# Kernel tuning notes

Measured on AMD Instinct MI355X. Metric: run time of the kernel, lower is better.

Reference implementation:

```python
import jax, jax.numpy as jnp
import numpy as np

N_NODES = 50000


def setup_inputs() -> dict:
    key = jax.random.key(0)
    ks = jax.random.split(key, 6)
    L, d = 3, 128
    x = jax.random.normal(ks[0], (N_NODES, d), dtype=jnp.float32)
    edge_index = jax.random.randint(ks[1], (2, 640000), 0, N_NODES, dtype=jnp.int64)
    s = 1.0 / np.sqrt(d)
    W1 = jax.random.normal(ks[2], (L, d, d), dtype=jnp.float32) * s
    W2 = jax.random.normal(ks[3], (L, d, d), dtype=jnp.float32) * s
    b1 = jnp.zeros((L, d), dtype=jnp.float32)
    b2 = jnp.zeros((L, d), dtype=jnp.float32)
    eps = jnp.zeros((L,), dtype=jnp.float32)
    final_w = jax.random.normal(ks[4], (d + L * d, d), dtype=jnp.float32) / np.sqrt(d + L * d)
    final_b = jnp.zeros((d,), dtype=jnp.float32)
    return {"x": x, "edge_index": edge_index, "W1": W1, "b1": b1,
            "W2": W2, "b2": b2, "eps": eps, "final_w": final_w, "final_b": final_b}


def reference(x, edge_index, W1, b1, W2, b2, eps, final_w, final_b):
    src, dst = edge_index[0], edge_index[1]
    num_layers = W1.shape[0]
    xs = [x]
    h = x
    for l in range(num_layers):
        # GINConv: sum-aggregate neighbor features, add (1+eps)*self, then 2-layer MLP
        agg = jax.ops.segment_sum(h[src], dst, num_segments=N_NODES)  # [N, d]
        z = (1.0 + eps[l]) * h + agg
        z = jax.nn.relu(z @ W1[l] + b1[l])
        h = jax.nn.relu(z @ W2[l] + b2[l])
        xs.append(h)
    out = jnp.concatenate(xs, axis=-1)  # [N, in + L*out]
    return out @ final_w + final_b
```

## Files before the change

kernel.cpp:

```cpp
#include <hip/hip_runtime.h>

#define NNODES 50000
#define NEDGES 640000
#define D 128

typedef unsigned short u16;
typedef unsigned int u32;
typedef __bf16 bf16x8 __attribute__((ext_vector_type(8)));
typedef float f32x4 __attribute__((ext_vector_type(4)));
union AB { uint4 u4; bf16x8 f; };

__device__ __forceinline__ u16 f2b(float f) {
    u32 u = __float_as_uint(f);
    return (u16)((u + 0x7fffu + ((u >> 16) & 1u)) >> 16);
}
__device__ __forceinline__ u32 pack2(float lo, float hi) {
    return (u32)f2b(lo) | ((u32)f2b(hi) << 16);
}
__device__ __forceinline__ float blo(u32 v) { return __uint_as_float(v << 16); }
__device__ __forceinline__ float bhi(u32 v) { return __uint_as_float(v & 0xffff0000u); }

__device__ __forceinline__ void acc8(float* a, uint4 v) {
    a[0] += blo(v.x); a[1] += bhi(v.x);
    a[2] += blo(v.y); a[3] += bhi(v.y);
    a[4] += blo(v.z); a[5] += bhi(v.z);
    a[6] += blo(v.w); a[7] += bhi(v.w);
}

__global__ void k_prep(const float* __restrict__ W1, const float* __restrict__ W2,
                       const float* __restrict__ fw, const float* __restrict__ x,
                       const int* __restrict__ dst,
                       u16* __restrict__ wT1, u16* __restrict__ wT2,
                       u16* __restrict__ fwTc, u32* __restrict__ xb,
                       int* __restrict__ cnt, int* __restrict__ epos) {
    int idx = blockIdx.x * 256 + threadIdx.x;
    if (idx < 3 * 16384) {
        int l = idx >> 14, r = idx & 16383, n = r >> 7, k = r & 127;
        wT1[idx] = f2b(W1[l * 16384 + k * 128 + n]);
        wT2[idx] = f2b(W2[l * 16384 + k * 128 + n]);
    }
    if (idx < 4 * 16384) {
        int ch = idx >> 14, r = idx & 16383, n = r >> 7, k = r & 127;
        fwTc[idx] = f2b(fw[(ch * 128 + k) * 128 + n]);
    }
    if (idx < NEDGES) {
        epos[idx] = atomicAdd(&cnt[dst[idx]], 1);
    }
    if (idx < NNODES * 64) {
        float2 v = ((const float2*)x)[idx];
        xb[idx] = pack2(v.x, v.y);
    }
}

__global__ void k_scan1(const int* __restrict__ cnt, int* __restrict__ rp,
                        int* __restrict__ bsum) {
    __shared__ int s[256];
    int tid = threadIdx.x;
    int i = blockIdx.x * 256 + tid;
    int v = (i < NNODES) ? cnt[i] : 0;
    s[tid] = v;
    __syncthreads();
    for (int off = 1; off < 256; off <<= 1) {
        int t = (tid >= off) ? s[tid - off] : 0;
        __syncthreads();
        s[tid] += t;
        __syncthreads();
    }
    if (i < NNODES) rp[i] = s[tid] - v;
    if (tid == 255) bsum[blockIdx.x] = s[255];
}

__global__ void k_scan2(int* __restrict__ bsum, int nb) {
    __shared__ int s[256];
    int tid = threadIdx.x;
    int v = (tid < nb) ? bsum[tid] : 0;
    s[tid] = v;
    __syncthreads();
    for (int off = 1; off < 256; off <<= 1) {
        int t = (tid >= off) ? s[tid - off] : 0;
        __syncthreads();
        s[tid] += t;
        __syncthreads();
    }
    if (tid < nb) bsum[tid] = s[tid] - v;
}

__global__ void k_add(int* __restrict__ rp, const int* __restrict__ bsum) {
    int i = blockIdx.x * 256 + threadIdx.x;
    if (i < NNODES) rp[i] += bsum[blockIdx.x];
    if (i == 0) rp[NNODES] = NEDGES;
}

__global__ void k_scatter(const int* __restrict__ src, const int* __restrict__ dst,
                          const int* __restrict__ rp, const int* __restrict__ epos,
                          int* __restrict__ srcs) {
    int e = blockIdx.x * 256 + threadIdx.x;
    if (e < NEDGES) srcs[rp[dst[e]] + epos[e]] = src[e];
}

__global__ void k_agg(const uint4* __restrict__ h4, const int* __restrict__ rp,
                      const int* __restrict__ srcs, const float* __restrict__ epsp,
                      uint4* __restrict__ z4) {
    int tid = threadIdx.x;
    int c = tid & 15;
    int node = (blockIdx.x * 256 + tid) >> 4;
    int gbase = tid & 48;
    float sc = 1.0f + epsp[0];

    uint4 sv = h4[node * 16 + c];
    float acc[8];
    acc[0] = sc * blo(sv.x); acc[1] = sc * bhi(sv.x);
    acc[2] = sc * blo(sv.y); acc[3] = sc * bhi(sv.y);
    acc[4] = sc * blo(sv.z); acc[5] = sc * bhi(sv.z);
    acc[6] = sc * blo(sv.w); acc[7] = sc * bhi(sv.w);

    int beg = rp[node], end = rp[node + 1];
    for (int base = beg; base < end; base += 16) {
        int n = end - base; if (n > 16) n = 16;
        int myidx = (base + c < end) ? srcs[base + c] : 0;
        int j = 0;
        for (; j + 8 <= n; j += 8) {
            int s0 = __shfl(myidx, gbase + j + 0, 64);
            int s1 = __shfl(myidx, gbase + j + 1, 64);
            int s2 = __shfl(myidx, gbase + j + 2, 64);
            int s3 = __shfl(myidx, gbase + j + 3, 64);
            int s4 = __shfl(myidx, gbase + j + 4, 64);
            int s5 = __shfl(myidx, gbase + j + 5, 64);
            int s6 = __shfl(myidx, gbase + j + 6, 64);
            int s7 = __shfl(myidx, gbase + j + 7, 64);
            uint4 v0 = h4[s0 * 16 + c]; uint4 v1 = h4[s1 * 16 + c];
            uint4 v2 = h4[s2 * 16 + c]; uint4 v3 = h4[s3 * 16 + c];
            uint4 v4 = h4[s4 * 16 + c]; uint4 v5 = h4[s5 * 16 + c];
            uint4 v6 = h4[s6 * 16 + c]; uint4 v7 = h4[s7 * 16 + c];
            acc8(acc, v0); acc8(acc, v1); acc8(acc, v2); acc8(acc, v3);
            acc8(acc, v4); acc8(acc, v5); acc8(acc, v6); acc8(acc, v7);
        }
        for (; j + 4 <= n; j += 4) {
            int s0 = __shfl(myidx, gbase + j + 0, 64);
            int s1 = __shfl(myidx, gbase + j + 1, 64);
            int s2 = __shfl(myidx, gbase + j + 2, 64);
            int s3 = __shfl(myidx, gbase + j + 3, 64);
            uint4 v0 = h4[s0 * 16 + c]; uint4 v1 = h4[s1 * 16 + c];
            uint4 v2 = h4[s2 * 16 + c]; uint4 v3 = h4[s3 * 16 + c];
            acc8(acc, v0); acc8(acc, v1); acc8(acc, v2); acc8(acc, v3);
        }
        for (; j < n; ++j) {
            int s0 = __shfl(myidx, gbase + j, 64);
            uint4 v0 = h4[s0 * 16 + c];
            acc8(acc, v0);
        }
    }

    uint4 o;
    o.x = pack2(acc[0], acc[1]); o.y = pack2(acc[2], acc[3]);
    o.z = pack2(acc[4], acc[5]); o.w = pack2(acc[6], acc[7]);
    z4[node * 16 + c] = o;
}

template <bool FINAL>
__launch_bounds__(256, 2)
__global__ void k_mlp(const u16* __restrict__ A, const u16* __restrict__ wT1g,
                      const float* __restrict__ b1, const u16* __restrict__ wT2g,
                      const float* __restrict__ b2, u16* __restrict__ H,
                      const u16* __restrict__ xbg, const u16* __restrict__ h1g,
                      const u16* __restrict__ h2g, const u16* __restrict__ fwTc,
                      const float* __restrict__ fb, float* __restrict__ out) {
    __shared__ u16 Tb[128 * 128];
    __shared__ u16 wbuf[128 * 128];
    uint4* Tb4 = (uint4*)Tb;
    uint4* wb4 = (uint4*)wbuf;
    int tid = threadIdx.x;
    int r0 = blockIdx.x * 128;
    int wave = tid >> 6, lane = tid & 63, l16 = lane & 15, quad = lane >> 4;

    {
        const uint4* g = (const uint4*)wT1g;
        for (int i = tid; i < 2048; i += 256) {
            int n = i >> 4, ch = i & 15;
            wb4[n * 16 + ((ch + n) & 15)] = g[i];
        }
    }

    AB a[2][4];
#pragma unroll
    for (int s = 0; s < 2; ++s) {
        int row = r0 + wave * 32 + s * 16 + l16;
#pragma unroll
        for (int kb = 0; kb < 4; ++kb) {
            if (row < NNODES)
                a[s][kb].u4 = *(const uint4*)&A[row * 128 + kb * 32 + quad * 8];
            else
                a[s][kb].u4 = make_uint4(0, 0, 0, 0);
        }
    }
    __syncthreads();

    f32x4 acc[2][8];
#pragma unroll
    for (int col = 0; col < 8; ++col) {
        float bv = b1[col * 16 + l16];
        acc[0][col] = (f32x4){bv, bv, bv, bv};
        acc[1][col] = (f32x4){bv, bv, bv, bv};
    }
#pragma unroll
    for (int col = 0; col < 8; ++col) {
#pragma unroll
        for (int kb = 0; kb < 4; ++kb) {
            AB b;
            int n = col * 16 + l16;
            b.u4 = wb4[n * 16 + ((kb * 4 + quad + n) & 15)];
            acc[0][col] = __builtin_amdgcn_mfma_f32_16x16x32_bf16(a[0][kb].f, b.f, acc[0][col], 0, 0, 0);
            acc[1][col] = __builtin_amdgcn_mfma_f32_16x16x32_bf16(a[1][kb].f, b.f, acc[1][col], 0, 0, 0);
        }
    }

#pragma unroll
    for (int s = 0; s < 2; ++s)
#pragma unroll
        for (int col = 0; col < 8; ++col)
#pragma unroll
            for (int r = 0; r < 4; ++r) {
                int row = wave * 32 + s * 16 + quad * 4 + r;
                int kcol = col * 16 + l16;
                int ch = kcol >> 3;
                Tb[row * 128 + ((ch + row) & 15) * 8 + (kcol & 7)] =
                    f2b(fmaxf(acc[s][col][r], 0.f));
            }
    __syncthreads();

    {
        const uint4* g = (const uint4*)wT2g;
        for (int i = tid; i < 2048; i += 256) {
            int n = i >> 4, ch = i & 15;
            wb4[n * 16 + ((ch + n) & 15)] = g[i];
        }
    }
    AB a2[2][4];
#pragma unroll
    for (int s = 0; s < 2; ++s) {
        int m = wave * 32 + s * 16 + l16;
#pragma unroll
        for (int kb = 0; kb < 4; ++kb)
            a2[s][kb].u4 = Tb4[m * 16 + ((kb * 4 + quad + m) & 15)];
    }
    __syncthreads();

#pragma unroll
    for (int col = 0; col < 8; ++col) {
        float bv = b2[col * 16 + l16];
        acc[0][col] = (f32x4){bv, bv, bv, bv};
        acc[1][col] = (f32x4){bv, bv, bv, bv};
    }
#pragma unroll
    for (int col = 0; col < 8; ++col) {
#pragma unroll
        for (int kb = 0; kb < 4; ++kb) {
            AB b;
            int n = col * 16 + l16;
            b.u4 = wb4[n * 16 + ((kb * 4 + quad + n) & 15)];
            acc[0][col] = __builtin_amdgcn_mfma_f32_16x16x32_bf16(a2[0][kb].f, b.f, acc[0][col], 0, 0, 0);
            acc[1][col] = __builtin_amdgcn_mfma_f32_16x16x32_bf16(a2[1][kb].f, b.f, acc[1][col], 0, 0, 0);
        }
    }

#pragma unroll
    for (int s = 0; s < 2; ++s)
#pragma unroll
        for (int col = 0; col < 8; ++col)
#pragma unroll
            for (int r = 0; r < 4; ++r) {
                int row = wave * 32 + s * 16 + quad * 4 + r;
                int kcol = col * 16 + l16;
                int ch = kcol >> 3;
                Tb[row * 128 + ((ch + row) & 15) * 8 + (kcol & 7)] =
                    f2b(fmaxf(acc[s][col][r], 0.f));
            }

    if constexpr (!FINAL) {
        __syncthreads();
        for (int i = tid; i < 2048; i += 256) {
            int r = i >> 4, ch = i & 15;
            int grow = r0 + r;
            if (grow < NNODES)
                *(uint4*)&H[grow * 128 + ch * 8] = Tb4[r * 16 + ((ch + r) & 15)];
        }
    } else {
#pragma unroll
        for (int col = 0; col < 8; ++col) {
            float bv = fb[col * 16 + l16];
            acc[0][col] = (f32x4){bv, bv, bv, bv};
            acc[1][col] = (f32x4){bv, bv, bv, bv};
        }
        const u16* chin[3] = {xbg, h1g, h2g};
        for (int chn = 0; chn < 4; ++chn) {
            __syncthreads();
            {
                const uint4* g = (const uint4*)(fwTc + chn * 16384);
                for (int i = tid; i < 2048; i += 256) {
                    int n = i >> 4, ch = i & 15;
                    wb4[n * 16 + ((ch + n) & 15)] = g[i];
                }
            }
            AB af[2][4];
            if (chn < 3) {
                const u16* cp = chin[chn];
#pragma unroll
                for (int s = 0; s < 2; ++s) {
                    int row = r0 + wave * 32 + s * 16 + l16;
#pragma unroll
                    for (int kb = 0; kb < 4; ++kb) {
                        if (row < NNODES)
                            af[s][kb].u4 = *(const uint4*)&cp[row * 128 + kb * 32 + quad * 8];
                        else
                            af[s][kb].u4 = make_uint4(0, 0, 0, 0);
                    }
                }
            } else {
#pragma unroll
                for (int s = 0; s < 2; ++s) {
                    int m = wave * 32 + s * 16 + l16;
#pragma unroll
                    for (int kb = 0; kb < 4; ++kb)
                        af[s][kb].u4 = Tb4[m * 16 + ((kb * 4 + quad + m) & 15)];
                }
            }
            __syncthreads();
#pragma unroll
            for (int col = 0; col < 8; ++col) {
#pragma unroll
                for (int kb = 0; kb < 4; ++kb) {
                    AB b;
                    int n = col * 16 + l16;
                    b.u4 = wb4[n * 16 + ((kb * 4 + quad + n) & 15)];
                    acc[0][col] = __builtin_amdgcn_mfma_f32_16x16x32_bf16(af[0][kb].f, b.f, acc[0][col], 0, 0, 0);
                    acc[1][col] = __builtin_amdgcn_mfma_f32_16x16x32_bf16(af[1][kb].f, b.f, acc[1][col], 0, 0, 0);
                }
            }
        }
#pragma unroll
        for (int s = 0; s < 2; ++s)
#pragma unroll
            for (int col = 0; col < 8; ++col)
#pragma unroll
                for (int r = 0; r < 4; ++r) {
                    int row = r0 + wave * 32 + s * 16 + quad * 4 + r;
                    if (row < NNODES) out[row * 128 + col * 16 + l16] = acc[s][col][r];
                }
    }
}

extern "C" void kernel_launch(void* const* d_in, const int* in_sizes, int n_in,
                              void* d_out, int out_size, void* d_ws, size_t ws_size,
                              hipStream_t stream) {
    const float* x   = (const float*)d_in[0];
    const int*   ei  = (const int*)d_in[1];
    const float* W1  = (const float*)d_in[2];
    const float* b1  = (const float*)d_in[3];
    const float* W2  = (const float*)d_in[4];
    const float* b2  = (const float*)d_in[5];
    const float* eps = (const float*)d_in[6];
    const float* fw  = (const float*)d_in[7];
    const float* fb  = (const float*)d_in[8];
    float* out = (float*)d_out;

    const int* srcA = ei;
    const int* dstA = ei + NEDGES;

    char* p = (char*)d_ws;
    size_t off = 0;
    auto take = [&](size_t bytes) {
        char* r = p + off;
        off = (off + bytes + 255) & ~(size_t)255;
        return r;
    };
    int* rp   = (int*)take((NNODES + 1) * sizeof(int));
    int* cnt  = (int*)take(NNODES * sizeof(int));
    int* bsum = (int*)take(256 * sizeof(int));
    int* epos = (int*)take(NEDGES * sizeof(int));
    int* srcs = (int*)take(NEDGES * sizeof(int));
    u16* wT1  = (u16*)take(3 * 16384 * sizeof(u16));
    u16* wT2  = (u16*)take(3 * 16384 * sizeof(u16));
    u16* fwTc = (u16*)take(4 * 16384 * sizeof(u16));
    u16* xb   = (u16*)take((size_t)NNODES * D * sizeof(u16));
    u16* zb   = (u16*)take((size_t)NNODES * D * sizeof(u16));
    u16* hb1  = (u16*)take((size_t)NNODES * D * sizeof(u16));
    u16* hb2  = (u16*)take((size_t)NNODES * D * sizeof(u16));
    (void)ws_size; (void)in_sizes; (void)n_in; (void)out_size;

    hipMemsetAsync(cnt, 0, NNODES * sizeof(int), stream);

    int nb = (NNODES + 255) / 256;
    k_prep<<<(NNODES * 64 + 255) / 256, 256, 0, stream>>>(W1, W2, fw, x, dstA,
                                                          wT1, wT2, fwTc, (u32*)xb,
                                                          cnt, epos);
    k_scan1<<<nb, 256, 0, stream>>>(cnt, rp, bsum);
    k_scan2<<<1, 256, 0, stream>>>(bsum, nb);
    k_add<<<nb, 256, 0, stream>>>(rp, bsum);
    k_scatter<<<(NEDGES + 255) / 256, 256, 0, stream>>>(srcA, dstA, rp, epos, srcs);

    int gm = (NNODES + 127) / 128;
    k_agg<<<NNODES * 16 / 256, 256, 0, stream>>>((const uint4*)xb, rp, srcs, eps + 0, (uint4*)zb);
    k_mlp<false><<<gm, 256, 0, stream>>>(zb, wT1, b1, wT2, b2, hb1,
                                         nullptr, nullptr, nullptr, nullptr, nullptr, nullptr);
    k_agg<<<NNODES * 16 / 256, 256, 0, stream>>>((const uint4*)hb1, rp, srcs, eps + 1, (uint4*)zb);
    k_mlp<false><<<gm, 256, 0, stream>>>(zb, wT1 + 16384, b1 + D, wT2 + 16384, b2 + D, hb2,
                                         nullptr, nullptr, nullptr, nullptr, nullptr, nullptr);
    k_agg<<<NNODES * 16 / 256, 256, 0, stream>>>((const uint4*)hb2, rp, srcs, eps + 2, (uint4*)zb);
    k_mlp<true><<<gm, 256, 0, stream>>>(zb, wT1 + 2 * 16384, b1 + 2 * D,
                                        wT2 + 2 * 16384, b2 + 2 * D, nullptr,
                                        xb, hb1, hb2, fwTc, fb, out);
}
```

Measured before the change: 262.9 us.

## Fuse scan kernels, vectorize bf16 prep, prefetch final-layer A chunks, add nontemporal hints

Merges the second-level scan into the first scan kernel: a last-block-done atomic counter (stored right after cnt) lets the final block scan the block sums, removing one launch. The prep kernel now converts four floats per thread instead of two, halving its grid, which still covers the edges and weights. The final MLP's concat projection prefetches the next input chunk into registers one step ahead so its loads overlap the MFMA work. Nontemporal loads and stores are added for edge indices, aggregated outputs and the final output, at the cost of extra register pressure and some reliance on cache-policy behaviour.

After: 269.0 us. +2.3%, slower.

```diff
diff --git a/kernel.cpp b/kernel.cpp
--- a/kernel.cpp
+++ b/kernel.cpp
@@ -8,6 +8,7 @@
 typedef unsigned int u32;
 typedef __bf16 bf16x8 __attribute__((ext_vector_type(8)));
 typedef float f32x4 __attribute__((ext_vector_type(4)));
+typedef u32 u32x4 __attribute__((ext_vector_type(4)));
 union AB { uint4 u4; bf16x8 f; };
 
 __device__ __forceinline__ u16 f2b(float f) {
@@ -31,7 +32,7 @@
                        const float* __restrict__ fw, const float* __restrict__ x,
                        const int* __restrict__ dst,
                        u16* __restrict__ wT1, u16* __restrict__ wT2,
-                       u16* __restrict__ fwTc, u32* __restrict__ xb,
+                       u16* __restrict__ fwTc, uint2* __restrict__ xb,
                        int* __restrict__ cnt, int* __restrict__ epos) {
     int idx = blockIdx.x * 256 + threadIdx.x;
     if (idx < 3 * 16384) {
@@ -46,15 +47,16 @@
     if (idx < NEDGES) {
         epos[idx] = atomicAdd(&cnt[dst[idx]], 1);
     }
-    if (idx < NNODES * 64) {
-        float2 v = ((const float2*)x)[idx];
-        xb[idx] = pack2(v.x, v.y);
+    if (idx < NNODES * 32) {
+        float4 v = ((const float4*)x)[idx];
+        xb[idx] = make_uint2(pack2(v.x, v.y), pack2(v.z, v.w));
     }
 }
 
 __global__ void k_scan1(const int* __restrict__ cnt, int* __restrict__ rp,
-                        int* __restrict__ bsum) {
+                        int* __restrict__ bsum, int* __restrict__ counter) {
     __shared__ int s[256];
+    __shared__ int lastBlk;
     int tid = threadIdx.x;
     int i = blockIdx.x * 256 + tid;
     int v = (i < NNODES) ? cnt[i] : 0;
@@ -67,22 +69,32 @@
         __syncthreads();
     }
     if (i < NNODES) rp[i] = s[tid] - v;
-    if (tid == 255) bsum[blockIdx.x] = s[255];
-}
-
-__global__ void k_scan2(int* __restrict__ bsum, int nb) {
-    __shared__ int s[256];
-    int tid = threadIdx.x;
-    int v = (tid < nb) ? bsum[tid] : 0;
-    s[tid] = v;
-    __syncthreads();
-    for (int off = 1; off < 256; off <<= 1) {
-        int t = (tid >= off) ? s[tid - off] : 0;
+    if (tid == 255)
+        __hip_atomic_store(&bsum[blockIdx.x], s[255], __ATOMIC_RELEASE,
+                           __HIP_MEMORY_SCOPE_AGENT);
+    __syncthreads();
+    if (tid == 0) {
+        int n = __hip_atomic_fetch_add(counter, 1, __ATOMIC_ACQ_REL,
+                                       __HIP_MEMORY_SCOPE_AGENT);
+        lastBlk = (n == (int)gridDim.x - 1);
+    }
+    __syncthreads();
+    if (lastBlk) {
+        int nb = gridDim.x;
+        int v2 = (tid < nb)
+                     ? __hip_atomic_load(&bsum[tid], __ATOMIC_ACQUIRE,
+                                         __HIP_MEMORY_SCOPE_AGENT)
+                     : 0;
+        s[tid] = v2;
         __syncthreads();
-        s[tid] += t;
-        __syncthreads();
-    }
-    if (tid < nb) bsum[tid] = s[tid] - v;
+        for (int off = 1; off < 256; off <<= 1) {
+            int t = (tid >= off) ? s[tid - off] : 0;
+            __syncthreads();
+            s[tid] += t;
+            __syncthreads();
+        }
+        if (tid < nb) bsum[tid] = s[tid] - v2;
+    }
 }
 
 __global__ void k_add(int* __restrict__ rp, const int* __restrict__ bsum) {
@@ -117,7 +129,8 @@
     int beg = rp[node], end = rp[node + 1];
     for (int base = beg; base < end; base += 16) {
         int n = end - base; if (n > 16) n = 16;
-        int myidx = (base + c < end) ? srcs[base + c] : 0;
+        int myidx = 0;
+        if (base + c < end) myidx = __builtin_nontemporal_load(srcs + base + c);
         int j = 0;
         for (; j + 8 <= n; j += 8) {
             int s0 = __shfl(myidx, gbase + j + 0, 64);
@@ -151,10 +164,10 @@
         }
     }
 
-    uint4 o;
+    u32x4 o;
     o.x = pack2(acc[0], acc[1]); o.y = pack2(acc[2], acc[3]);
     o.z = pack2(acc[4], acc[5]); o.w = pack2(acc[6], acc[7]);
-    z4[node * 16 + c] = o;
+    __builtin_nontemporal_store(o, (u32x4*)&z4[node * 16 + c]);
 }
 
 template <bool FINAL>
@@ -292,6 +305,17 @@
             acc[1][col] = (f32x4){bv, bv, bv, bv};
         }
         const u16* chin[3] = {xbg, h1g, h2g};
+        AB afN[2][4];
+#pragma unroll
+        for (int s = 0; s < 2; ++s) {
+            int row = r0 + wave * 32 + s * 16 + l16;
+#pragma unroll
+            for (int kb = 0; kb < 4; ++kb)
+                afN[s][kb].u4 = (row < NNODES)
+                                    ? *(const uint4*)&xbg[row * 128 + kb * 32 + quad * 8]
+                                    : make_uint4(0, 0, 0, 0);
+        }
+#pragma unroll
         for (int chn = 0; chn < 4; ++chn) {
             __syncthreads();
             {
@@ -302,26 +326,28 @@
                 }
             }
             AB af[2][4];
-            if (chn < 3) {
-                const u16* cp = chin[chn];
+#pragma unroll
+            for (int s = 0; s < 2; ++s)
+#pragma unroll
+                for (int kb = 0; kb < 4; ++kb) af[s][kb] = afN[s][kb];
+            if (chn < 2) {
+                const u16* cp = chin[chn + 1];
 #pragma unroll
                 for (int s = 0; s < 2; ++s) {
                     int row = r0 + wave * 32 + s * 16 + l16;
 #pragma unroll
-                    for (int kb = 0; kb < 4; ++kb) {
-                        if (row < NNODES)
-                            af[s][kb].u4 = *(const uint4*)&cp[row * 128 + kb * 32 + quad * 8];
-                        else
-                            af[s][kb].u4 = make_uint4(0, 0, 0, 0);
-                    }
+                    for (int kb = 0; kb < 4; ++kb)
+                        afN[s][kb].u4 = (row < NNODES)
+                                            ? *(const uint4*)&cp[row * 128 + kb * 32 + quad * 8]
+                                            : make_uint4(0, 0, 0, 0);
                 }
-            } else {
+            } else if (chn == 2) {
 #pragma unroll
                 for (int s = 0; s < 2; ++s) {
                     int m = wave * 32 + s * 16 + l16;
 #pragma unroll
                     for (int kb = 0; kb < 4; ++kb)
-                        af[s][kb].u4 = Tb4[m * 16 + ((kb * 4 + quad + m) & 15)];
+                        afN[s][kb].u4 = Tb4[m * 16 + ((kb * 4 + quad + m) & 15)];
                 }
             }
             __syncthreads();
@@ -344,7 +370,9 @@
 #pragma unroll
                 for (int r = 0; r < 4; ++r) {
                     int row = r0 + wave * 32 + s * 16 + quad * 4 + r;
-                    if (row < NNODES) out[row * 128 + col * 16 + l16] = acc[s][col][r];
+                    if (row < NNODES)
+                        __builtin_nontemporal_store(acc[s][col][r],
+                                                    &out[row * 128 + col * 16 + l16]);
                 }
     }
 }
@@ -374,7 +402,7 @@
         return r;
     };
     int* rp   = (int*)take((NNODES + 1) * sizeof(int));
-    int* cnt  = (int*)take(NNODES * sizeof(int));
+    int* cnt  = (int*)take((NNODES + 1) * sizeof(int));
     int* bsum = (int*)take(256 * sizeof(int));
     int* epos = (int*)take(NEDGES * sizeof(int));
     int* srcs = (int*)take(NEDGES * sizeof(int));
@@ -387,14 +415,13 @@
     u16* hb2  = (u16*)take((size_t)NNODES * D * sizeof(u16));
     (void)ws_size; (void)in_sizes; (void)n_in; (void)out_size;
 
-    hipMemsetAsync(cnt, 0, NNODES * sizeof(int), stream);
+    (void)hipMemsetAsync(cnt, 0, (NNODES + 1) * sizeof(int), stream);
 
     int nb = (NNODES + 255) / 256;
-    k_prep<<<(NNODES * 64 + 255) / 256, 256, 0, stream>>>(W1, W2, fw, x, dstA,
-                                                          wT1, wT2, fwTc, (u32*)xb,
+    k_prep<<<(NNODES * 32 + 255) / 256, 256, 0, stream>>>(W1, W2, fw, x, dstA,
+                                                          wT1, wT2, fwTc, (uint2*)xb,
                                                           cnt, epos);
-    k_scan1<<<nb, 256, 0, stream>>>(cnt, rp, bsum);
-    k_scan2<<<1, 256, 0, stream>>>(bsum, nb);
+    k_scan1<<<nb, 256, 0, stream>>>(cnt, rp, bsum, cnt + NNODES);
     k_add<<<nb, 256, 0, stream>>>(rp, bsum);
     k_scatter<<<(NEDGES + 255) / 256, 256, 0, stream>>>(srcA, dstA, rp, epos, srcs);
 
```
